# Kernel optimization log

Hardware: AMD Instinct MI355X
Metric: run time of the kernel (lower is better)

## Reference

```python
import jax, jax.numpy as jnp
import numpy as np

MAX_TAG = 16          # tag ids live in [0, MAX_TAG]; 0 = background
NUM_SEG = MAX_TAG + 1
LGG_VALUE = 3.0


def setup_inputs() -> dict:
    key = jax.random.key(0)
    k1, k2, k3 = jax.random.split(key, 3)
    B, C, H, W = 16, 8, 512, 512
    gt_kernel_key = jax.random.randint(k1, (B, H, W), 0, MAX_TAG + 1, dtype=jnp.int32)
    training_mask = jax.random.randint(k2, (B, H, W), 0, 2, dtype=jnp.int32)
    similarity_vector = jax.random.normal(k3, (B, C, H, W), dtype=jnp.float32)
    return {
        "gt_kernel_key": gt_kernel_key,
        "training_mask": training_mask,
        "similarity_vector": similarity_vector,
    }


def _per_sample_loss(sim_hwc, gk, mask):
    # sim_hwc: [H, W, C]; gk, mask: [H, W]
    C = sim_hwc.shape[-1]
    flat_sim = sim_hwc.reshape(-1, C)            # [HW, C]
    flat_gk = gk.reshape(-1)                     # [HW]
    ones = jnp.ones_like(flat_gk, dtype=jnp.float32)

    # segment mean per tag over the UNMASKED kernel map (matches original:
    # tags are selected with the mask, but means use gt_kernel directly)
    sums = jax.ops.segment_sum(flat_sim, flat_gk, num_segments=NUM_SEG)      # [T, C]
    counts = jax.ops.segment_sum(ones, flat_gk, num_segments=NUM_SEG)       # [T]
    means = sums / jnp.maximum(counts, 1.0)[:, None]

    # a tag participates iff it appears in gt_kernel_key * training_mask and != 0
    masked_gk = flat_gk * mask.reshape(-1)
    masked_counts = jax.ops.segment_sum(ones, masked_gk, num_segments=NUM_SEG)
    present = (masked_counts > 0).at[0].set(False)                           # [T]

    # pairwise distances between tag means (tiny: NUM_SEG x NUM_SEG)
    diff = means[:, None, :] - means[None, :, :]                             # [T, T, C]
    dist = jnp.sqrt(jnp.sum(diff * diff, axis=-1) + 1e-12)                   # [T, T]
    pair_loss = jnp.log(jnp.maximum(LGG_VALUE - dist, 0.0) ** 2 + 1.0)

    valid = present[:, None] & present[None, :] & ~jnp.eye(NUM_SEG, dtype=bool)
    n_valid = jnp.sum(valid.astype(jnp.float32))
    loss = jnp.sum(jnp.where(valid, pair_loss, 0.0)) / jnp.maximum(n_valid, 1.0)
    sample_valid = (jnp.sum(present.astype(jnp.int32)) >= 2).astype(jnp.float32)
    return loss, sample_valid


def reference(gt_kernel_key, training_mask, similarity_vector):
    # [B, C, H, W] -> [B, H, W, C]
    sim = jnp.transpose(similarity_vector, (0, 2, 3, 1))
    losses, valids = jax.vmap(_per_sample_loss)(sim, gt_kernel_key, training_mask)
    n = jnp.sum(valids)
    return jnp.where(n > 0, jnp.sum(losses * valids) / jnp.maximum(n, 1.0), 0.0)
```

## Files before the change

### kernel.cpp

```cpp
#include <hip/hip_runtime.h>

#define NB 16
#define NC 8
#define HW (512*512)
#define NT 16
#define LGG 3.0f

#define BLOCKS 2048
#define THREADS 256
#define BPSAMP (BLOCKS/NB)
#define PXB (HW/BPSAMP)
#define PXW (PXB/4)
#define NMFMA (PXW/32)

typedef __attribute__((ext_vector_type(8))) short bf16x8;
typedef __attribute__((ext_vector_type(4))) float f32x4;


__device__ __forceinline__ unsigned pk_bf16(float x, float y) {
    unsigned r;
    asm("v_cvt_pk_bf16_f32 %0, %1, %2" : "=v"(r) : "v"(x), "v"(y));
    return r;
}

__global__ __launch_bounds__(THREADS) void accum(
    const int* __restrict__ gk, const int* __restrict__ mask,
    const float* __restrict__ sim,
    float* __restrict__ psum, unsigned* __restrict__ ppb)
{
    const int tid  = threadIdx.x;
    const int lane = tid & 63, wid = tid >> 6;
    const int bid  = blockIdx.x;
    const int b    = bid / BPSAMP;
    const int sb   = bid % BPSAMP;
    const int c    = lane & 15;
    const int l4   = lane >> 4;
    const int p0   = sb * PXB + wid * PXW + l4 * 8;

    const int*   gkp = gk   + (size_t)b * HW + p0;
    const int*   mkp = mask + (size_t)b * HW + p0;
    const float* sp  = sim  + ((size_t)b * NC + c) * HW + p0;

    __shared__ float    lred[4][256];
    __shared__ unsigned s_pb;
    if (tid == 0) s_pb = 0u;
    __syncthreads();

    f32x4 acc = {0.f, 0.f, 0.f, 0.f};
    unsigned pb = 0u;
    const int r1 = c + 1;

    #pragma unroll 1
    for (int it = 0; it < NMFMA; ++it) {
        const int off = it * 32;
        const int4 g0 = *(const int4*)(gkp + off);
        const int4 g1 = *(const int4*)(gkp + off + 4);

        union { bf16x8 v; unsigned u[4]; } A;
        A.u[0] = (g0.x == r1 ? 0x3F80u : 0u) | (g0.y == r1 ? 0x3F800000u : 0u);
        A.u[1] = (g0.z == r1 ? 0x3F80u : 0u) | (g0.w == r1 ? 0x3F800000u : 0u);
        A.u[2] = (g1.x == r1 ? 0x3F80u : 0u) | (g1.y == r1 ? 0x3F800000u : 0u);
        A.u[3] = (g1.z == r1 ? 0x3F80u : 0u) | (g1.w == r1 ? 0x3F800000u : 0u);

        union { bf16x8 v; unsigned u[4]; } B;
        if (c < 8) {
            const float4 v0 = *(const float4*)(sp + off);
            const float4 v1 = *(const float4*)(sp + off + 4);
            B.u[0] = pk_bf16(v0.x, v0.y); B.u[1] = pk_bf16(v0.z, v0.w);
            B.u[2] = pk_bf16(v1.x, v1.y); B.u[3] = pk_bf16(v1.z, v1.w);
        } else if (c == 8) {
            B.u[0] = B.u[1] = B.u[2] = B.u[3] = 0x3F803F80u;
        } else {
            B.u[0] = B.u[1] = B.u[2] = B.u[3] = 0u;
            if (c == 9) {
                const int4 m0 = *(const int4*)(mkp + off);
                const int4 m1 = *(const int4*)(mkp + off + 4);
                if (m0.x) pb |= 1u << g0.x;
                if (m0.y) pb |= 1u << g0.y;
                if (m0.z) pb |= 1u << g0.z;
                if (m0.w) pb |= 1u << g0.w;
                if (m1.x) pb |= 1u << g1.x;
                if (m1.y) pb |= 1u << g1.y;
                if (m1.z) pb |= 1u << g1.z;
                if (m1.w) pb |= 1u << g1.w;
            }
        }

        acc = __builtin_amdgcn_mfma_f32_16x16x32_bf16(A.v, B.v, acc, 0, 0, 0);
    }

    const int row0 = (lane >> 4) * 4;
    #pragma unroll
    for (int i = 0; i < 4; ++i) lred[wid][(row0 + i) * 16 + c] = acc[i];
    if (c == 9) atomicOr(&s_pb, pb);
    __syncthreads();

    if (tid < NT * 9) {
        const int r = tid / 9, cc = tid % 9;
        const float s = lred[0][r*16+cc] + lred[1][r*16+cc]
                      + lred[2][r*16+cc] + lred[3][r*16+cc];
        psum[(size_t)bid * 144 + tid] = s;
    }
    if (tid == 0) ppb[bid] = s_pb;
}

__global__ __launch_bounds__(256) void reduce_sample(
    const float* __restrict__ psum, const unsigned* __restrict__ ppb,
    float* __restrict__ sout)
{
    const int b = blockIdx.x, tid = threadIdx.x;
    __shared__ float    S[144];
    __shared__ float    cnts[NT];
    __shared__ float    means[NT][NC];
    __shared__ unsigned s_pres;
    __shared__ float    lsum[4], lnv[4];
    if (tid == 0) s_pres = 0u;
    __syncthreads();

    if (tid < 144) {
        float s = 0.f;
        for (int i = 0; i < BPSAMP; ++i)
            s += psum[(size_t)(b * BPSAMP + i) * 144 + tid];
        S[tid] = s;
    }
    {
        unsigned u = (tid < BPSAMP) ? ppb[b * BPSAMP + tid] : 0u;
        #pragma unroll
        for (int o = 32; o; o >>= 1) u |= __shfl_xor(u, o);
        if ((tid & 63) == 0) atomicOr(&s_pres, u);
    }
    __syncthreads();
    if (tid < NT) cnts[tid] = S[tid * 9 + 8];
    __syncthreads();
    if (tid < NT * NC)
        means[tid >> 3][tid & 7] = S[(tid >> 3) * 9 + (tid & 7)]
                                   / fmaxf(cnts[tid >> 3], 1.f);
    __syncthreads();

    const unsigned pres = s_pres & 0x1FFFEu;
    const int i = tid >> 4, j = tid & 15;
    float loss = 0.f, nv = 0.f;
    if (i != j && ((pres >> (i + 1)) & 1u) && ((pres >> (j + 1)) & 1u)) {
        float d2 = 0.f;
        #pragma unroll
        for (int cc = 0; cc < NC; ++cc) {
            const float d = means[i][cc] - means[j][cc];
            d2 += d * d;
        }
        const float dist = sqrtf(d2 + 1e-12f);
        const float r = fmaxf(LGG - dist, 0.f);
        loss = logf(r * r + 1.f);
        nv = 1.f;
    }
    #pragma unroll
    for (int o = 32; o; o >>= 1) { loss += __shfl_xor(loss, o); nv += __shfl_xor(nv, o); }
    if ((tid & 63) == 0) { lsum[tid >> 6] = loss; lnv[tid >> 6] = nv; }
    __syncthreads();
    if (tid == 0) {
        const float tl = lsum[0] + lsum[1] + lsum[2] + lsum[3];
        const float tn = lnv[0] + lnv[1] + lnv[2] + lnv[3];
        const float v = (__popc(pres) >= 2) ? 1.f : 0.f;
        sout[b]      = v * (tl / fmaxf(tn, 1.f));
        sout[NB + b] = v;
    }
}

__global__ __launch_bounds__(64) void final_k(
    const float* __restrict__ sout, float* __restrict__ out)
{
    const int tid = threadIdx.x;
    float l = (tid < NB) ? sout[tid]      : 0.f;
    float v = (tid < NB) ? sout[NB + tid] : 0.f;
    #pragma unroll
    for (int o = 32; o; o >>= 1) { l += __shfl_xor(l, o); v += __shfl_xor(v, o); }
    if (tid == 0) out[0] = (v > 0.f) ? l / v : 0.f;
}

extern "C" void kernel_launch(void* const* d_in, const int* in_sizes, int n_in,
                              void* d_out, int out_size, void* d_ws, size_t ws_size,
                              hipStream_t stream) {
    const int*   gk   = (const int*)d_in[0];
    const int*   mask = (const int*)d_in[1];
    const float* sim  = (const float*)d_in[2];
    float* out = (float*)d_out;

    float*    psum = (float*)d_ws;
    unsigned* ppb  = (unsigned*)(psum + BLOCKS * 144);
    float*    sout = (float*)(ppb + BLOCKS);

    accum<<<BLOCKS, THREADS, 0, stream>>>(gk, mask, sim, psum, ppb);
    reduce_sample<<<NB, 256, 0, stream>>>(psum, ppb, sout);
    final_k<<<1, 64, 0, stream>>>(sout, out);
}
```

Measured before the change: 55.44 us.

## Fold mask presence into MFMA column and reduce partials via global atomics

The per-lane bitmask OR for tag presence is replaced by a tenth MFMA column holding the training-mask indicator, so masked counts come out of the same matrix multiply. Per-block partial sums are added atomically into a small per-sample workspace instead of being written out and reduced by a separate per-sample kernel. The per-sample reduction and the final kernel are merged into one single-block finalize kernel, and a zero-init kernel is added. The aim is to remove the 2048x144 partial write and re-read and a launch, at the cost of global float atomic contention (128 blocks per sample hit the same 160 addresses) and nondeterministic summation order. The loop unroll also goes from 1 to 2.

Measured after the change: 54.71 us. About the same (-1.3%).

```diff
diff --git a/kernel.cpp b/kernel.cpp
--- a/kernel.cpp
+++ b/kernel.cpp
@@ -12,6 +12,8 @@
 #define PXB (HW/BPSAMP)
 #define PXW (PXB/4)
 #define NMFMA (PXW/32)
+#define NCOL 10
+#define ACCW (NT*NCOL)
 
 typedef __attribute__((ext_vector_type(8))) short bf16x8;
 typedef __attribute__((ext_vector_type(4))) float f32x4;
@@ -23,10 +25,16 @@
     return r;
 }
 
+__global__ __launch_bounds__(256) void init_ws(float* g_acc) {
+    const int i = threadIdx.x;
+    #pragma unroll
+    for (int k = 0; k < NB*ACCW; k += 256)
+        if (k + i < NB*ACCW) g_acc[k + i] = 0.f;
+}
+
 __global__ __launch_bounds__(THREADS) void accum(
     const int* __restrict__ gk, const int* __restrict__ mask,
-    const float* __restrict__ sim,
-    float* __restrict__ psum, unsigned* __restrict__ ppb)
+    const float* __restrict__ sim, float* __restrict__ g_acc)
 {
     const int tid  = threadIdx.x;
     const int lane = tid & 63, wid = tid >> 6;
@@ -41,16 +49,12 @@
     const int*   mkp = mask + (size_t)b * HW + p0;
     const float* sp  = sim  + ((size_t)b * NC + c) * HW + p0;
 
-    __shared__ float    lred[4][256];
-    __shared__ unsigned s_pb;
-    if (tid == 0) s_pb = 0u;
-    __syncthreads();
+    __shared__ float lred[4][256];
 
     f32x4 acc = {0.f, 0.f, 0.f, 0.f};
-    unsigned pb = 0u;
     const int r1 = c + 1;
 
-    #pragma unroll 1
+    #pragma unroll 2
     for (int it = 0; it < NMFMA; ++it) {
         const int off = it * 32;
         const int4 g0 = *(const int4*)(gkp + off);
@@ -70,20 +74,15 @@
             B.u[2] = pk_bf16(v1.x, v1.y); B.u[3] = pk_bf16(v1.z, v1.w);
         } else if (c == 8) {
             B.u[0] = B.u[1] = B.u[2] = B.u[3] = 0x3F803F80u;
+        } else if (c == 9) {
+            const int4 m0 = *(const int4*)(mkp + off);
+            const int4 m1 = *(const int4*)(mkp + off + 4);
+            B.u[0] = (m0.x ? 0x3F80u : 0u) | (m0.y ? 0x3F800000u : 0u);
+            B.u[1] = (m0.z ? 0x3F80u : 0u) | (m0.w ? 0x3F800000u : 0u);
+            B.u[2] = (m1.x ? 0x3F80u : 0u) | (m1.y ? 0x3F800000u : 0u);
+            B.u[3] = (m1.z ? 0x3F80u : 0u) | (m1.w ? 0x3F800000u : 0u);
         } else {
             B.u[0] = B.u[1] = B.u[2] = B.u[3] = 0u;
-            if (c == 9) {
-                const int4 m0 = *(const int4*)(mkp + off);
-                const int4 m1 = *(const int4*)(mkp + off + 4);
-                if (m0.x) pb |= 1u << g0.x;
-                if (m0.y) pb |= 1u << g0.y;
-                if (m0.z) pb |= 1u << g0.z;
-                if (m0.w) pb |= 1u << g0.w;
-                if (m1.x) pb |= 1u << g1.x;
-                if (m1.y) pb |= 1u << g1.y;
-                if (m1.z) pb |= 1u << g1.z;
-                if (m1.w) pb |= 1u << g1.w;
-            }
         }
 
         acc = __builtin_amdgcn_mfma_f32_16x16x32_bf16(A.v, B.v, acc, 0, 0, 0);
@@ -92,88 +91,72 @@
     const int row0 = (lane >> 4) * 4;
     #pragma unroll
     for (int i = 0; i < 4; ++i) lred[wid][(row0 + i) * 16 + c] = acc[i];
-    if (c == 9) atomicOr(&s_pb, pb);
     __syncthreads();
 
-    if (tid < NT * 9) {
-        const int r = tid / 9, cc = tid % 9;
+    if (tid < NT * NCOL) {
+        const int r = tid / NCOL, cc = tid % NCOL;
         const float s = lred[0][r*16+cc] + lred[1][r*16+cc]
                       + lred[2][r*16+cc] + lred[3][r*16+cc];
-        psum[(size_t)bid * 144 + tid] = s;
-    }
-    if (tid == 0) ppb[bid] = s_pb;
-}
-
-__global__ __launch_bounds__(256) void reduce_sample(
-    const float* __restrict__ psum, const unsigned* __restrict__ ppb,
-    float* __restrict__ sout)
-{
-    const int b = blockIdx.x, tid = threadIdx.x;
-    __shared__ float    S[144];
-    __shared__ float    cnts[NT];
-    __shared__ float    means[NT][NC];
-    __shared__ unsigned s_pres;
-    __shared__ float    lsum[4], lnv[4];
-    if (tid == 0) s_pres = 0u;
-    __syncthreads();
-
-    if (tid < 144) {
-        float s = 0.f;
-        for (int i = 0; i < BPSAMP; ++i)
-            s += psum[(size_t)(b * BPSAMP + i) * 144 + tid];
-        S[tid] = s;
-    }
-    {
-        unsigned u = (tid < BPSAMP) ? ppb[b * BPSAMP + tid] : 0u;
-        #pragma unroll
-        for (int o = 32; o; o >>= 1) u |= __shfl_xor(u, o);
-        if ((tid & 63) == 0) atomicOr(&s_pres, u);
-    }
-    __syncthreads();
-    if (tid < NT) cnts[tid] = S[tid * 9 + 8];
-    __syncthreads();
-    if (tid < NT * NC)
-        means[tid >> 3][tid & 7] = S[(tid >> 3) * 9 + (tid & 7)]
-                                   / fmaxf(cnts[tid >> 3], 1.f);
-    __syncthreads();
-
-    const unsigned pres = s_pres & 0x1FFFEu;
-    const int i = tid >> 4, j = tid & 15;
-    float loss = 0.f, nv = 0.f;
-    if (i != j && ((pres >> (i + 1)) & 1u) && ((pres >> (j + 1)) & 1u)) {
-        float d2 = 0.f;
-        #pragma unroll
-        for (int cc = 0; cc < NC; ++cc) {
-            const float d = means[i][cc] - means[j][cc];
-            d2 += d * d;
-        }
-        const float dist = sqrtf(d2 + 1e-12f);
-        const float r = fmaxf(LGG - dist, 0.f);
-        loss = logf(r * r + 1.f);
-        nv = 1.f;
-    }
-    #pragma unroll
-    for (int o = 32; o; o >>= 1) { loss += __shfl_xor(loss, o); nv += __shfl_xor(nv, o); }
-    if ((tid & 63) == 0) { lsum[tid >> 6] = loss; lnv[tid >> 6] = nv; }
-    __syncthreads();
-    if (tid == 0) {
-        const float tl = lsum[0] + lsum[1] + lsum[2] + lsum[3];
-        const float tn = lnv[0] + lnv[1] + lnv[2] + lnv[3];
-        const float v = (__popc(pres) >= 2) ? 1.f : 0.f;
-        sout[b]      = v * (tl / fmaxf(tn, 1.f));
-        sout[NB + b] = v;
+        atomicAdd(&g_acc[b * ACCW + tid], s);
     }
 }
 
-__global__ __launch_bounds__(64) void final_k(
-    const float* __restrict__ sout, float* __restrict__ out)
+__global__ __launch_bounds__(256) void finalize(
+    const float* __restrict__ g_acc, float* __restrict__ out)
 {
+    __shared__ float    means[NB][NT][NC];
+    __shared__ unsigned pres[NB];
+    __shared__ float    sl[NB], sn[NB];
     const int tid = threadIdx.x;
-    float l = (tid < NB) ? sout[tid]      : 0.f;
-    float v = (tid < NB) ? sout[NB + tid] : 0.f;
+
+    if (tid < NB) pres[tid] = 0u;
+    __syncthreads();
+
+    {
+        const int b = tid >> 4, t = tid & 15;
+        const float* row = g_acc + b * ACCW + t * NCOL;
+        const float cnt = row[8];
+        const float mc  = row[9];
+        const float inv = 1.f / fmaxf(cnt, 1.f);
+        #pragma unroll
+        for (int cc = 0; cc < NC; ++cc) means[b][t][cc] = row[cc] * inv;
+        if (mc > 0.5f) atomicOr(&pres[b], 1u << (t + 1));
+    }
+    __syncthreads();
+
+    const int b = tid >> 4, i = tid & 15;
+    const unsigned pr = pres[b];
+    float loss = 0.f, nv = 0.f;
+    if ((pr >> (i + 1)) & 1u) {
+        #pragma unroll
+        for (int j = 0; j < NT; ++j) {
+            if (j != i && ((pr >> (j + 1)) & 1u)) {
+                float d2 = 0.f;
+                #pragma unroll
+                for (int cc = 0; cc < NC; ++cc) {
+                    const float d = means[b][i][cc] - means[b][j][cc];
+                    d2 += d * d;
+                }
+                const float dist = sqrtf(d2 + 1e-12f);
+                const float r = fmaxf(LGG - dist, 0.f);
+                loss += logf(r * r + 1.f);
+                nv += 1.f;
+            }
+        }
+    }
     #pragma unroll
-    for (int o = 32; o; o >>= 1) { l += __shfl_xor(l, o); v += __shfl_xor(v, o); }
-    if (tid == 0) out[0] = (v > 0.f) ? l / v : 0.f;
+    for (int o = 8; o; o >>= 1) { loss += __shfl_xor(loss, o); nv += __shfl_xor(nv, o); }
+    if (i == 0) {
+        const float v = (__popc(pr) >= 2) ? 1.f : 0.f;
+        sl[b] = v * (loss / fmaxf(nv, 1.f));
+        sn[b] = v;
+    }
+    __syncthreads();
+    if (tid == 0) {
+        float tl = 0.f, tv = 0.f;
+        for (int bb = 0; bb < NB; ++bb) { tl += sl[bb]; tv += sn[bb]; }
+        out[0] = (tv > 0.f) ? tl / tv : 0.f;
+    }
 }
 
 extern "C" void kernel_launch(void* const* d_in, const int* in_sizes, int n_in,
@@ -182,13 +165,10 @@
     const int*   gk   = (const int*)d_in[0];
     const int*   mask = (const int*)d_in[1];
     const float* sim  = (const float*)d_in[2];
-    float* out = (float*)d_out;
+    float* out   = (float*)d_out;
+    float* g_acc = (float*)d_ws;
 
-    float*    psum = (float*)d_ws;
-    unsigned* ppb  = (unsigned*)(psum + BLOCKS * 144);
-    float*    sout = (float*)(ppb + BLOCKS);
-
-    accum<<<BLOCKS, THREADS, 0, stream>>>(gk, mask, sim, psum, ppb);
-    reduce_sample<<<NB, 256, 0, stream>>>(psum, ppb, sout);
-    final_k<<<1, 64, 0, stream>>>(sout, out);
+    init_ws<<<1, 256, 0, stream>>>(g_acc);
+    accum<<<BLOCKS, THREADS, 0, stream>>>(gk, mask, sim, g_acc);
+    finalize<<<1, 256, 0, stream>>>(g_acc, out);
 }
```
